# Performance work log

Hardware: AMD Instinct MI355X
Metric: run time of the kernel (lower is better)

The kernel has to match this reference:

```python
import jax, jax.numpy as jnp
import numpy as np

DIM = 192
HEADS = 6
HEAD_DIM = 32
WS = 7          # window_size
DISP = WS // 2  # cyclic-shift displacement = 3
NEG = -1e9      # large negative instead of -inf (grad-safe, numerically equivalent)


def _rel_indices():
    idx = np.array([[x, y] for x in range(WS) for y in range(WS)])  # [WS^2, 2]
    d = idx[None, :, :] - idx[:, None, :] + WS - 1                  # [WS^2, WS^2, 2]
    return d


def _shift_masks():
    n = WS * WS
    ul = np.zeros((n, n), dtype=np.float32)
    ul[-DISP * WS:, :-DISP * WS] = NEG
    ul[:-DISP * WS, -DISP * WS:] = NEG
    lr = np.zeros((WS, WS, WS, WS), dtype=np.float32)
    lr[:, -DISP:, :, :-DISP] = NEG
    lr[:, :-DISP, :, -DISP:] = NEG
    lr = lr.reshape(n, n)
    return ul, lr


def setup_inputs() -> dict:
    key = jax.random.key(0)
    k1, k2, k3, k4, k5 = jax.random.split(key, 5)
    inner = HEADS * HEAD_DIM
    B, H, W = 32, 56, 56
    x = jax.random.normal(k1, (B, H, W, DIM), dtype=jnp.float32)
    w_qkv = jax.random.normal(k2, (DIM, inner * 3), dtype=jnp.float32) * (DIM ** -0.5)
    w_out = jax.random.normal(k3, (inner, DIM), dtype=jnp.float32) * (inner ** -0.5)
    b_out = jnp.zeros((DIM,), dtype=jnp.float32)
    pos_emb = jax.random.normal(k4, (2 * WS - 1, 2 * WS - 1), dtype=jnp.float32)
    return {"x": x, "w_qkv": w_qkv, "w_out": w_out, "b_out": b_out, "pos_emb": pos_emb}


def _forward(x, w_qkv, w_out, b_out, pos_emb):
    b, n_h, n_w, _ = x.shape
    nw_h, nw_w = n_h // WS, n_w // WS
    nw = nw_h * nw_w
    n = WS * WS
    scale = HEAD_DIM ** -0.5

    # cyclic shift
    x = jnp.roll(x, shift=(-DISP, -DISP), axis=(1, 2))

    qkv = x @ w_qkv  # [b, H, W, 3*inner]
    qkv = qkv.reshape(b, nw_h, WS, nw_w, WS, 3, HEADS, HEAD_DIM)
    # -> [3, b, heads, nw, WS*WS, head_dim]
    qkv = qkv.transpose(5, 0, 6, 1, 3, 2, 4, 7).reshape(3, b, HEADS, nw, n, HEAD_DIM)
    q, k, v = qkv[0], qkv[1], qkv[2]

    dots = jnp.einsum('bhwid,bhwjd->bhwij', q, k) * scale  # [b,h,nw,n,n]

    rel = _rel_indices()
    bias = pos_emb[rel[:, :, 0], rel[:, :, 1]]  # [n, n]
    dots = dots + bias

    # shifted-window masks: last row of windows gets UL mask, last column gets LR mask
    ul, lr = _shift_masks()
    madd = jnp.zeros((nw, n, n), dtype=dots.dtype)
    madd = madd.at[-nw_w:].add(jnp.asarray(ul))
    madd = madd.at[nw_w - 1::nw_w].add(jnp.asarray(lr))
    dots = dots + madd

    attn = jax.nn.softmax(dots, axis=-1)
    out = jnp.einsum('bhwij,bhwjd->bhwid', attn, v)  # [b,h,nw,n,hd]

    # un-window: -> [b, H, W, inner]
    out = out.reshape(b, HEADS, nw_h, nw_w, WS, WS, HEAD_DIM)
    out = out.transpose(0, 2, 4, 3, 5, 1, 6).reshape(b, n_h, n_w, HEADS * HEAD_DIM)
    out = out @ w_out + b_out

    # cyclic back-shift
    out = jnp.roll(out, shift=(DISP, DISP), axis=(1, 2))
    return out


def reference(x, w_qkv, w_out, b_out, pos_emb):
    return _forward(x, w_qkv, w_out, b_out, pos_emb)
```

## Files before the change

### kernel.cpp

```cpp
#include <hip/hip_runtime.h>
#include <hip/hip_bf16.h>


typedef __bf16 bf16x8 __attribute__((ext_vector_type(8)));
typedef float f32x4 __attribute__((ext_vector_type(4)));
using bf = __bf16;

#define MFMA16(a, b, c) __builtin_amdgcn_mfma_f32_16x16x32_bf16((a), (b), (c), 0, 0, 0)

static constexpr float kNEG = -1000000000.0f;
static constexpr float kScale = 0.17677669529663687f;

static constexpr size_t OFF_WQKVT = 0;
static constexpr size_t OFF_WOUTT = 221184;
static constexpr size_t OFF_TBL   = 294912;

static constexpr int QK_STRIDE = 40;
static constexpr int VT_STRIDE = 72;
static constexpr int X_STRIDE  = 200;
static constexpr int O_STRIDE  = 200;
static constexpr int P_STRIDE  = 72;
static constexpr int R0_OFF = 0;
static constexpr int R1_OFF = 23552;
static constexpr int R2_OFF = 47104;
static constexpr int LDS_BYTES = R2_OFF + 27648;

__device__ __forceinline__ unsigned pack2(float a, float b) {
  union { bf h[2]; unsigned u; } cv;
  cv.h[0] = (bf)a; cv.h[1] = (bf)b;
  return cv.u;
}

__global__ void prep_kernel(const float* __restrict__ wqkv, const float* __restrict__ wout,
                            const float* __restrict__ pos, char* __restrict__ ws) {
  bf* wqkvT = (bf*)(ws + OFF_WQKVT);
  bf* woutT = (bf*)(ws + OFF_WOUTT);
  float* tbl = (float*)(ws + OFF_TBL);
  int tid = blockIdx.x * blockDim.x + threadIdx.x;
  int nthr = gridDim.x * blockDim.x;
  for (int i = tid; i < 192 * 576; i += nthr) {
    int k = i / 576, n = i % 576;
    wqkvT[n * 192 + k] = (bf)wqkv[i];
  }
  for (int i = tid; i < 192 * 192; i += nthr) {
    int k = i / 192, n = i % 192;
    woutT[n * 192 + k] = (bf)wout[i];
  }
  for (int i = tid; i < 4 * 64 * 64; i += nthr) {
    int type = i >> 12, rem = i & 4095, r = rem >> 6, c = rem & 63;
    float v;
    if (r < 49 && c < 49) {
      int ix = r / 7, iy = r % 7, jx = c / 7, jy = c % 7;
      v = pos[(jx - ix + 6) * 13 + (jy - iy + 6)];
      if ((type & 1) && ((r >= 28) != (c >= 28))) v += kNEG;
      if ((type & 2) && ((iy >= 4) != (jy >= 4))) v += kNEG;
    } else {
      v = kNEG;
    }
    tbl[i] = v;
  }
}

__global__ __launch_bounds__(512, 4) void fused_kernel(const float* __restrict__ x,
                                                       const float* __restrict__ bout,
                                                       const char* __restrict__ ws,
                                                       float* __restrict__ out) {
  __shared__ __align__(16) char smem[LDS_BYTES];
  bf* Xl = (bf*)(smem + R0_OFF);
  bf* Ql = (bf*)(smem + R0_OFF);
  bf* Pl = (bf*)(smem + R0_OFF);
  bf* Kl = (bf*)(smem + R1_OFF);
  bf* Ol = (bf*)(smem + R1_OFF);
  bf* Vl = (bf*)(smem + R2_OFF);

  const bf* wqkvT = (const bf*)(ws + OFF_WQKVT);
  const bf* woutT = (const bf*)(ws + OFF_WOUTT);

  int bw = blockIdx.x;
  int b = bw >> 6, win = bw & 63;
  int wh = win >> 3, wwi = win & 7;
  int type = ((wh == 7) ? 1 : 0) | ((wwi == 7) ? 2 : 0);
  const float* tbl = (const float*)(ws + OFF_TBL) + type * 4096;

  int tid = threadIdx.x;
  int wave = tid >> 6, lane = tid & 63;
  int l15 = lane & 15, g = lane >> 4;
  int mrow = wave >> 2, ncol = wave & 3;

#pragma unroll
  for (int it = 0; it < 3; ++it) {
    int chunk = it * 512 + tid;
    if (chunk < 1176) {
      int r = chunk / 24, c8 = (chunk % 24) * 8;
      int tr = r / 7, tc = r % 7;
      int h = wh * 7 + tr + 3; if (h >= 56) h -= 56;
      int w = wwi * 7 + tc + 3; if (w >= 56) w -= 56;
      const float* p = x + (((size_t)b * 56 + h) * 56 + w) * 192 + c8;
      bf16x8 v;
#pragma unroll
      for (int j = 0; j < 8; ++j) v[j] = (bf)p[j];
      *(bf16x8*)(Xl + r * X_STRIDE + c8) = v;
    }
  }
  __syncthreads();

  f32x4 acc[2][9] = {};
#pragma unroll
  for (int ks = 0; ks < 6; ++ks) {
    bf16x8 a[2];
#pragma unroll
    for (int mt = 0; mt < 2; ++mt) {
      int t = mrow * 32 + mt * 16 + l15; if (t > 48) t = 48;
      a[mt] = *(const bf16x8*)(Xl + t * X_STRIDE + ks * 32 + g * 8);
    }
#pragma unroll
    for (int nt = 0; nt < 9; ++nt) {
      bf16x8 bfr = *(const bf16x8*)(wqkvT + (size_t)(ncol * 144 + nt * 16 + l15) * 192 + ks * 32 + g * 8);
#pragma unroll
      for (int mt = 0; mt < 2; ++mt) acc[mt][nt] = MFMA16(a[mt], bfr, acc[mt][nt]);
    }
  }
  __syncthreads();

#pragma unroll
  for (int nt = 0; nt < 9; ++nt) {
    int n = ncol * 144 + nt * 16 + l15;
    int s3 = n / 192;
    int hd = (n % 192) >> 5;
    int d = n & 31;
#pragma unroll
    for (int mt = 0; mt < 2; ++mt) {
#pragma unroll
      for (int r = 0; r < 4; ++r) {
        int t = mrow * 32 + mt * 16 + 4 * g + r;
        bf bv = (bf)acc[mt][nt][r];
        if (s3 == 0)      { if (t < 49) Ql[(hd * 49 + t) * QK_STRIDE + d] = bv; }
        else if (s3 == 1) { if (t < 49) Kl[(hd * 49 + t) * QK_STRIDE + d] = bv; }
        else              { Vl[(hd * 32 + d) * VT_STRIDE + t] = bv; }
      }
    }
  }
  __syncthreads();

  unsigned pp[3][8];
#pragma unroll
  for (int ii = 0; ii < 3; ++ii) {
    int item = wave + ii * 8;
    int head = item >> 2, mq = item & 3;
    const bf* Qh = Ql + head * 49 * QK_STRIDE;
    const bf* Kh = Kl + head * 49 * QK_STRIDE;

    int tq = mq * 16 + l15; if (tq > 48) tq = 48;
    bf16x8 qf = *(const bf16x8*)(Qh + tq * QK_STRIDE + g * 8);
    f32x4 sa[4];
#pragma unroll
    for (int nt = 0; nt < 4; ++nt) {
      int tk = nt * 16 + l15; if (tk > 48) tk = 48;
      bf16x8 kf = *(const bf16x8*)(Kh + tk * QK_STRIDE + g * 8);
      f32x4 z = {};
      sa[nt] = MFMA16(qf, kf, z);
    }
#pragma unroll
    for (int nt = 0; nt < 4; ++nt)
#pragma unroll
      for (int r = 0; r < 4; ++r)
        sa[nt][r] = sa[nt][r] * kScale + tbl[(mq * 16 + 4 * g + r) * 64 + nt * 16 + l15];

#pragma unroll
    for (int r = 0; r < 4; ++r) {
      float m = fmaxf(fmaxf(sa[0][r], sa[1][r]), fmaxf(sa[2][r], sa[3][r]));
#pragma unroll
      for (int off = 1; off < 16; off <<= 1) m = fmaxf(m, __shfl_xor(m, off));
      float p0 = __expf(sa[0][r] - m), p1 = __expf(sa[1][r] - m);
      float p2 = __expf(sa[2][r] - m), p3 = __expf(sa[3][r] - m);
      float sum = p0 + p1 + p2 + p3;
#pragma unroll
      for (int off = 1; off < 16; off <<= 1) sum += __shfl_xor(sum, off);
      float rinv = 1.0f / sum;
      pp[ii][r * 2]     = pack2(p0 * rinv, p1 * rinv);
      pp[ii][r * 2 + 1] = pack2(p2 * rinv, p3 * rinv);
    }
  }
  __syncthreads();

  bf* Pw = Pl + wave * 16 * P_STRIDE;
  for (int ii = 0; ii < 3; ++ii) {
    int item = wave + ii * 8;
    int head = item >> 2, mq = item & 3;
    const bf* Vh = Vl + head * 32 * VT_STRIDE;

#pragma unroll
    for (int r = 0; r < 4; ++r) {
      int prow = 4 * g + r;
      union { unsigned u; bf h[2]; } ua, ub;
      ua.u = pp[ii][r * 2]; ub.u = pp[ii][r * 2 + 1];
      Pw[prow * P_STRIDE + l15]      = ua.h[0];
      Pw[prow * P_STRIDE + 16 + l15] = ua.h[1];
      Pw[prow * P_STRIDE + 32 + l15] = ub.h[0];
      Pw[prow * P_STRIDE + 48 + l15] = ub.h[1];
    }
    asm volatile("s_waitcnt lgkmcnt(0)" ::: "memory");
    __builtin_amdgcn_sched_barrier(0);

    f32x4 o0 = {}, o1 = {};
#pragma unroll
    for (int ks = 0; ks < 2; ++ks) {
      bf16x8 pf = *(const bf16x8*)(Pw + l15 * P_STRIDE + ks * 32 + g * 8);
      bf16x8 v0 = *(const bf16x8*)(Vh + l15 * VT_STRIDE + ks * 32 + g * 8);
      bf16x8 v1 = *(const bf16x8*)(Vh + (16 + l15) * VT_STRIDE + ks * 32 + g * 8);
      o0 = MFMA16(pf, v0, o0);
      o1 = MFMA16(pf, v1, o1);
    }
#pragma unroll
    for (int r = 0; r < 4; ++r) {
      int orow = mq * 16 + 4 * g + r;
      if (orow < 49) {
        Ol[orow * O_STRIDE + head * 32 + l15]      = (bf)o0[r];
        Ol[orow * O_STRIDE + head * 32 + 16 + l15] = (bf)o1[r];
      }
    }
    asm volatile("s_waitcnt lgkmcnt(0)" ::: "memory");
    __builtin_amdgcn_sched_barrier(0);
  }
  __syncthreads();

  f32x4 pacc[2][3] = {};
#pragma unroll
  for (int ks = 0; ks < 6; ++ks) {
    int t0 = mrow * 32 + l15;      if (t0 > 48) t0 = 48;
    int t1 = mrow * 32 + 16 + l15; if (t1 > 48) t1 = 48;
    bf16x8 a0 = *(const bf16x8*)(Ol + t0 * O_STRIDE + ks * 32 + g * 8);
    bf16x8 a1 = *(const bf16x8*)(Ol + t1 * O_STRIDE + ks * 32 + g * 8);
#pragma unroll
    for (int nt = 0; nt < 3; ++nt) {
      bf16x8 bfr = *(const bf16x8*)(woutT + (size_t)(ncol * 48 + nt * 16 + l15) * 192 + ks * 32 + g * 8);
      pacc[0][nt] = MFMA16(a0, bfr, pacc[0][nt]);
      pacc[1][nt] = MFMA16(a1, bfr, pacc[1][nt]);
    }
  }
#pragma unroll
  for (int nt = 0; nt < 3; ++nt) {
    int col = ncol * 48 + nt * 16 + l15;
    float bo = bout[col];
#pragma unroll
    for (int mt = 0; mt < 2; ++mt) {
#pragma unroll
      for (int r = 0; r < 4; ++r) {
        int t = mrow * 32 + mt * 16 + 4 * g + r;
        if (t < 49) {
          int tr = t / 7, tc = t % 7;
          int h = wh * 7 + tr + 3; if (h >= 56) h -= 56;
          int w2 = wwi * 7 + tc + 3; if (w2 >= 56) w2 -= 56;
          out[(((size_t)b * 56 + h) * 56 + w2) * 192 + col] = pacc[mt][nt][r] + bo;
        }
      }
    }
  }
}

extern "C" void kernel_launch(void* const* d_in, const int* in_sizes, int n_in,
                              void* d_out, int out_size, void* d_ws, size_t ws_size,
                              hipStream_t stream) {
  const float* x = (const float*)d_in[0];
  const float* wqkv = (const float*)d_in[1];
  const float* wout = (const float*)d_in[2];
  const float* bout = (const float*)d_in[3];
  const float* pos = (const float*)d_in[4];
  char* ws = (char*)d_ws;

  hipLaunchKernelGGL(prep_kernel, dim3(128), dim3(256), 0, stream, wqkv, wout, pos, ws);
  hipLaunchKernelGGL(fused_kernel, dim3(2048), dim3(512), 0, stream,
                     x, bout, (const char*)ws, (float*)d_out);
}
```

Measured before the change: 192.9 us.

## Split QKV projection into K/V then Q passes and stage bias table in LDS

```diff
diff --git a/kernel.cpp b/kernel.cpp
--- a/kernel.cpp
+++ b/kernel.cpp
@@ -3,6 +3,7 @@
 
 
 typedef __bf16 bf16x8 __attribute__((ext_vector_type(8)));
+typedef __bf16 bf16x4 __attribute__((ext_vector_type(4)));
 typedef float f32x4 __attribute__((ext_vector_type(4)));
 using bf = __bf16;
 
@@ -20,10 +21,12 @@
 static constexpr int X_STRIDE  = 200;
 static constexpr int O_STRIDE  = 200;
 static constexpr int P_STRIDE  = 72;
+static constexpr int TB_STRIDE = 68;
 static constexpr int R0_OFF = 0;
 static constexpr int R1_OFF = 23552;
 static constexpr int R2_OFF = 47104;
-static constexpr int LDS_BYTES = R2_OFF + 27648;
+static constexpr int TB_OFF = 74752;
+static constexpr int LDS_BYTES = TB_OFF + 49 * TB_STRIDE * 2 + 8;
 
 __device__ __forceinline__ unsigned pack2(float a, float b) {
   union { bf h[2]; unsigned u; } cv;
@@ -72,6 +75,7 @@
   bf* Kl = (bf*)(smem + R1_OFF);
   bf* Ol = (bf*)(smem + R1_OFF);
   bf* Vl = (bf*)(smem + R2_OFF);
+  bf* Tb = (bf*)(smem + TB_OFF);
 
   const bf* wqkvT = (const bf*)(ws + OFF_WQKVT);
   const bf* woutT = (const bf*)(ws + OFF_WOUTT);
@@ -80,7 +84,7 @@
   int b = bw >> 6, win = bw & 63;
   int wh = win >> 3, wwi = win & 7;
   int type = ((wh == 7) ? 1 : 0) | ((wwi == 7) ? 2 : 0);
-  const float* tbl = (const float*)(ws + OFF_TBL) + type * 4096;
+  const float* tblg = (const float*)(ws + OFF_TBL) + type * 4096;
 
   int tid = threadIdx.x;
   int wave = tid >> 6, lane = tid & 63;
@@ -102,41 +106,84 @@
       *(bf16x8*)(Xl + r * X_STRIDE + c8) = v;
     }
   }
+  if (tid < 392) {
+    int r = tid >> 3, c8 = (tid & 7) * 8;
+    const float* p = tblg + r * 64 + c8;
+    bf16x4 v0, v1;
+#pragma unroll
+    for (int j = 0; j < 4; ++j) { v0[j] = (bf)p[j]; v1[j] = (bf)p[4 + j]; }
+    *(bf16x4*)(Tb + r * TB_STRIDE + c8) = v0;
+    *(bf16x4*)(Tb + r * TB_STRIDE + c8 + 4) = v1;
+  }
   __syncthreads();
 
-  f32x4 acc[2][9] = {};
-#pragma unroll
-  for (int ks = 0; ks < 6; ++ks) {
-    bf16x8 a[2];
-#pragma unroll
-    for (int mt = 0; mt < 2; ++mt) {
-      int t = mrow * 32 + mt * 16 + l15; if (t > 48) t = 48;
-      a[mt] = *(const bf16x8*)(Xl + t * X_STRIDE + ks * 32 + g * 8);
-    }
-#pragma unroll
-    for (int nt = 0; nt < 9; ++nt) {
-      bf16x8 bfr = *(const bf16x8*)(wqkvT + (size_t)(ncol * 144 + nt * 16 + l15) * 192 + ks * 32 + g * 8);
-#pragma unroll
-      for (int mt = 0; mt < 2; ++mt) acc[mt][nt] = MFMA16(a[mt], bfr, acc[mt][nt]);
-    }
-  }
-  __syncthreads();
-
-#pragma unroll
-  for (int nt = 0; nt < 9; ++nt) {
-    int n = ncol * 144 + nt * 16 + l15;
-    int s3 = n / 192;
-    int hd = (n % 192) >> 5;
-    int d = n & 31;
-#pragma unroll
-    for (int mt = 0; mt < 2; ++mt) {
-#pragma unroll
-      for (int r = 0; r < 4; ++r) {
-        int t = mrow * 32 + mt * 16 + 4 * g + r;
-        bf bv = (bf)acc[mt][nt][r];
-        if (s3 == 0)      { if (t < 49) Ql[(hd * 49 + t) * QK_STRIDE + d] = bv; }
-        else if (s3 == 1) { if (t < 49) Kl[(hd * 49 + t) * QK_STRIDE + d] = bv; }
-        else              { Vl[(hd * 32 + d) * VT_STRIDE + t] = bv; }
+  {
+    f32x4 acc[2][6] = {};
+#pragma unroll
+    for (int ks = 0; ks < 6; ++ks) {
+      bf16x8 a[2];
+#pragma unroll
+      for (int mt = 0; mt < 2; ++mt) {
+        int t = mrow * 32 + mt * 16 + l15; if (t > 48) t = 48;
+        a[mt] = *(const bf16x8*)(Xl + t * X_STRIDE + ks * 32 + g * 8);
+      }
+#pragma unroll
+      for (int nt = 0; nt < 6; ++nt) {
+        int n = 192 + ncol * 96 + nt * 16 + l15;
+        bf16x8 bfr = *(const bf16x8*)(wqkvT + (size_t)n * 192 + ks * 32 + g * 8);
+#pragma unroll
+        for (int mt = 0; mt < 2; ++mt) acc[mt][nt] = MFMA16(a[mt], bfr, acc[mt][nt]);
+      }
+    }
+#pragma unroll
+    for (int nt = 0; nt < 6; ++nt) {
+      int n = 192 + ncol * 96 + nt * 16 + l15;
+      int s3 = n / 192;
+      int lc = n - s3 * 192;
+      int hd = lc >> 5, d = lc & 31;
+#pragma unroll
+      for (int mt = 0; mt < 2; ++mt) {
+#pragma unroll
+        for (int r = 0; r < 4; ++r) {
+          int t = mrow * 32 + mt * 16 + 4 * g + r;
+          bf bv = (bf)acc[mt][nt][r];
+          if (s3 == 1) { if (t < 49) Kl[(hd * 49 + t) * QK_STRIDE + d] = bv; }
+          else         { Vl[(hd * 32 + d) * VT_STRIDE + t] = bv; }
+        }
+      }
+    }
+  }
+
+  {
+    f32x4 qacc[2][3] = {};
+#pragma unroll
+    for (int ks = 0; ks < 6; ++ks) {
+      bf16x8 a[2];
+#pragma unroll
+      for (int mt = 0; mt < 2; ++mt) {
+        int t = mrow * 32 + mt * 16 + l15; if (t > 48) t = 48;
+        a[mt] = *(const bf16x8*)(Xl + t * X_STRIDE + ks * 32 + g * 8);
+      }
+#pragma unroll
+      for (int nt = 0; nt < 3; ++nt) {
+        int n = ncol * 48 + nt * 16 + l15;
+        bf16x8 bfr = *(const bf16x8*)(wqkvT + (size_t)n * 192 + ks * 32 + g * 8);
+#pragma unroll
+        for (int mt = 0; mt < 2; ++mt) qacc[mt][nt] = MFMA16(a[mt], bfr, qacc[mt][nt]);
+      }
+    }
+    __syncthreads();
+#pragma unroll
+    for (int nt = 0; nt < 3; ++nt) {
+      int n = ncol * 48 + nt * 16 + l15;
+      int hd = n >> 5, d = n & 31;
+#pragma unroll
+      for (int mt = 0; mt < 2; ++mt) {
+#pragma unroll
+        for (int r = 0; r < 4; ++r) {
+          int t = mrow * 32 + mt * 16 + 4 * g + r;
+          if (t < 49) Ql[(hd * 49 + t) * QK_STRIDE + d] = (bf)qacc[mt][nt][r];
+        }
       }
     }
   }
@@ -161,10 +208,13 @@
       sa[nt] = MFMA16(qf, kf, z);
     }
 #pragma unroll
-    for (int nt = 0; nt < 4; ++nt)
-#pragma unroll
-      for (int r = 0; r < 4; ++r)
-        sa[nt][r] = sa[nt][r] * kScale + tbl[(mq * 16 + 4 * g + r) * 64 + nt * 16 + l15];
+    for (int r = 0; r < 4; ++r) {
+      int rowc = mq * 16 + 4 * g + r; if (rowc > 48) rowc = 48;
+      const bf* trow = Tb + rowc * TB_STRIDE + l15;
+#pragma unroll
+      for (int nt = 0; nt < 4; ++nt)
+        sa[nt][r] = sa[nt][r] * kScale + (float)trow[nt * 16];
+    }
 
 #pragma unroll
     for (int r = 0; r < 4; ++r) {
```

Measured after the change: 180.0 us. 6.7% less time.
